# Kernel tuning notes

Measured on AMD Instinct MI355X. Metric: run time of the kernel, lower is better.

## Reference

```python
import jax, jax.numpy as jnp
import numpy as np

B, T, D, M, L = 4, 2048, 256, 128, 16
P = M * L  # max_pair_cnt


def setup_inputs() -> dict:
    key = jax.random.key(0)
    ks = jax.random.split(key, 11)
    head = jax.random.normal(ks[0], (B, P, T), jnp.float32) * 0.05
    tail = jax.random.normal(ks[1], (B, P, T), jnp.float32) * 0.05
    x = jax.random.normal(ks[2], (B, T, D), jnp.float32)
    coref_mention_position = jax.random.uniform(ks[3], (B, M, T), jnp.float32)
    lab = jax.random.uniform(ks[4], (B, P, 2), jnp.float32) + 1e-3
    coref_label = lab / lab.sum(-1, keepdims=True)  # already-softmaxed target
    coref_label_mask = jax.random.randint(ks[5], (B, P), 0, 2).astype(bool)
    lens = jnp.full((B, M), L, jnp.int32)  # uniform segment lengths
    w1 = jax.random.normal(ks[6], (3 * D, D), jnp.float32) / np.sqrt(3 * D).astype(np.float32)
    b1 = jnp.zeros((D,), jnp.float32)
    w2 = jax.random.normal(ks[7], (D, 2), jnp.float32) / np.sqrt(D).astype(np.float32)
    b2 = jnp.zeros((2,), jnp.float32)
    return {"head": head, "tail": tail, "lens": lens, "x": x,
            "coref_mention_position": coref_mention_position,
            "coref_label": coref_label, "coref_label_mask": coref_label_mask,
            "w1": w1, "b1": b1, "w2": w2, "b2": b2}


def reference(head, tail, lens, x, coref_mention_position, coref_label,
              coref_label_mask, w1, b1, w2, b2):
    # bmm-based gather of mention reps: [B,P,T] @ [B,T,D] -> [B,P,D]
    head_rep = jnp.einsum('bpt,btd->bpd', head, x)
    tail_rep = jnp.einsum('bpt,btd->bpd', tail, x)
    feat = jnp.concatenate([head_rep, tail_rep, head_rep * tail_rep], axis=-1)
    logits = jax.nn.relu(feat @ w1 + b1) @ w2 + b2  # [B,P,2]

    # ragged split_n_pad -> per-mention top-1 select (uniform lens == L -> reshape)
    scores = logits[..., 1].reshape(B, M, L)            # [B,M,L]
    max_idx = jnp.argmax(scores, axis=-1)               # [B,M]
    max_val = jnp.max(scores, axis=-1)                  # [B,M] (raw logit, as in source)
    tail_seg = tail_rep.reshape(B, M, L, D)
    sel = jnp.take_along_axis(tail_seg, max_idx[:, :, None, None], axis=2)[:, :, 0, :]
    coref_rep_m = sel * max_val[:, :, None]             # [B,M,D]

    # scatter-bmm merge back into sequence: [B,T,M] @ [B,M,D] -> [B,T,D]
    coref_rep = jnp.einsum('bmt,bmd->btd', coref_mention_position, coref_rep_m)
    output = x + coref_rep

    # KLDivLoss(reduction='mean') over masked pairs
    logq = jax.nn.log_softmax(logits, axis=-1)
    lab = coref_label
    pw = jnp.where(lab > 0, lab * jnp.log(jnp.maximum(lab, 1e-38)), 0.0) - lab * logq
    n = jnp.sum(coref_label_mask).astype(jnp.float32)
    loss = jnp.where(coref_label_mask[..., None], pw, 0.0).sum() / (n * 2.0)
    return output, loss
```

## Files before the change

kernel.cpp:

```cpp
#include <hip/hip_runtime.h>
#include <hip/hip_bf16.h>
#include <stdint.h>

#define TAU 0.35f

typedef __attribute__((ext_vector_type(8))) short bf16x8;
typedef __attribute__((ext_vector_type(4))) float f32x4;

__device__ __forceinline__ unsigned short f2bf(float f) {
  __bf16 h = (__bf16)f;
  return __builtin_bit_cast(unsigned short, h);
}
__device__ __forceinline__ float bf2f(unsigned short u) {
  unsigned int v = ((unsigned int)u) << 16;
  return __builtin_bit_cast(float, v);
}
__device__ __forceinline__ void async_copy16(const void* g, void* l) {
  __builtin_amdgcn_global_load_lds(
      (const __attribute__((address_space(1))) unsigned int*)g,
      (__attribute__((address_space(3))) unsigned int*)l, 16, 0, 0);
}

__global__ __launch_bounds__(256) void k_prep(
    const float* __restrict__ x, const float* __restrict__ w1,
    const float* __restrict__ b2,
    unsigned short* __restrict__ xt, unsigned short* __restrict__ w1t,
    float* __restrict__ logits, int* __restrict__ njobs) {
  __shared__ float tileS[64][65];
  int bx = blockIdx.x, tid = threadIdx.x;
  if (bx == 0 && tid == 0) *njobs = 0;
  if (bx < 64) {
    int i = bx * 256 + tid;
    logits[i] = b2[i & 1];
  }
  int j = tid & 63, i0 = tid >> 6;
  if (bx < 512) {
    int b = bx >> 7, t6 = (bx >> 2) & 31, d6 = bx & 3;
    const float* src = x + ((size_t)b * 2048 + (size_t)t6 * 64) * 256 + d6 * 64;
    for (int i = i0; i < 64; i += 4) tileS[i][j] = src[(size_t)i * 256 + j];
    __syncthreads();
    unsigned short* dst = xt + ((size_t)b * 256 + (size_t)d6 * 64) * 2048 + t6 * 64;
    for (int r = i0; r < 64; r += 4) dst[(size_t)r * 2048 + j] = f2bf(tileS[j][r]);
  } else {
    int wt = bx - 512;
    int k6 = wt >> 2, n6 = wt & 3;
    const float* src = w1 + ((size_t)k6 * 64) * 256 + n6 * 64;
    for (int i = i0; i < 64; i += 4) tileS[i][j] = src[(size_t)i * 256 + j];
    __syncthreads();
    unsigned short* dst = w1t + ((size_t)n6 * 64) * 768 + k6 * 64;
    for (int r = i0; r < 64; r += 4) dst[(size_t)r * 768 + j] = f2bf(tileS[j][r]);
  }
}

__global__ __launch_bounds__(256, 4) void k_gemm_rep(
    const float* __restrict__ head, const float* __restrict__ tail,
    const unsigned short* __restrict__ xt,
    float* __restrict__ hrep, float* __restrict__ trep) {
  __shared__ unsigned short As[2][4096];
  __shared__ unsigned short Bs[2][4096];
  int bx = blockIdx.x;
  int ntile = bx >> 8;
  int g = bx & 255;
  int b = g >> 6, mtile = g & 63;
  const float* Asrc = ((mtile < 32) ? head : tail) +
                      ((size_t)(b * 2048 + (mtile & 31) * 64)) * 2048;
  float* Crep = (mtile < 32) ? hrep : trep;
  const unsigned short* Bsrc = xt + ((size_t)(b * 256 + ntile * 64)) * 2048;

  int tid = threadIdx.x, lane = tid & 63, w = tid >> 6;

  int arow = tid >> 2, akq = tid & 3;
  const float* aptr = Asrc + (size_t)arow * 2048 + akq * 16;
  int rt = arow >> 4, r15 = arow & 15;
  int k8a = akq * 2, k8b = akq * 2 + 1;
  int awi0 = rt * 128 + (k8a >> 2) * 64 + (k8a & 3) * 16 + r15;
  int awi1 = rt * 128 + (k8b >> 2) * 64 + (k8b & 3) * 16 + r15;

  const unsigned short* bg[2];
  int bdst[2];
#pragma unroll
  for (int a = 0; a < 2; ++a) {
    int colofs = a * 8 + (lane >> 3);
    int k8 = (lane & 7) ^ (colofs & 7);
    bg[a] = Bsrc + (size_t)(w * 16 + colofs) * 2048 + k8 * 8;
    bdst[a] = (w * 128 + a * 64 + lane) * 8;
  }

  int sw0 = (lane >> 4) ^ (lane & 7);
  int sw1 = (4 + (lane >> 4)) ^ (lane & 7);
  int colc[4];
#pragma unroll
  for (int ct = 0; ct < 4; ++ct) colc[ct] = (ct * 16 + (lane & 15)) * 8;

  f32x4 acc[4];
#pragma unroll
  for (int ct = 0; ct < 4; ++ct) acc[ct] = (f32x4){0.f, 0.f, 0.f, 0.f};

  float4 av[4];
  {
    const float4* ap = (const float4*)aptr;
    av[0] = ap[0]; av[1] = ap[1]; av[2] = ap[2]; av[3] = ap[3];
  }
#pragma unroll
  for (int a = 0; a < 2; ++a) { async_copy16(bg[a], &Bs[0][bdst[a]]); bg[a] += 64; }
  {
    bf16x8 p0, p1;
    p0[0] = (short)f2bf(av[0].x); p0[1] = (short)f2bf(av[0].y);
    p0[2] = (short)f2bf(av[0].z); p0[3] = (short)f2bf(av[0].w);
    p0[4] = (short)f2bf(av[1].x); p0[5] = (short)f2bf(av[1].y);
    p0[6] = (short)f2bf(av[1].z); p0[7] = (short)f2bf(av[1].w);
    p1[0] = (short)f2bf(av[2].x); p1[1] = (short)f2bf(av[2].y);
    p1[2] = (short)f2bf(av[2].z); p1[3] = (short)f2bf(av[2].w);
    p1[4] = (short)f2bf(av[3].x); p1[5] = (short)f2bf(av[3].y);
    p1[6] = (short)f2bf(av[3].z); p1[7] = (short)f2bf(av[3].w);
    *(bf16x8*)&As[0][awi0 * 8] = p0;
    *(bf16x8*)&As[0][awi1 * 8] = p1;
  }
  {
    const float4* ap = (const float4*)(aptr + 64);
    av[0] = ap[0]; av[1] = ap[1]; av[2] = ap[2]; av[3] = ap[3];
  }
  __syncthreads();

  for (int it = 0; it < 32; ++it) {
    int cur = it & 1, nxt = cur ^ 1;
    if (it < 31) {
#pragma unroll
      for (int a = 0; a < 2; ++a) { async_copy16(bg[a], &Bs[nxt][bdst[a]]); bg[a] += 64; }
      bf16x8 p0, p1;
      p0[0] = (short)f2bf(av[0].x); p0[1] = (short)f2bf(av[0].y);
      p0[2] = (short)f2bf(av[0].z); p0[3] = (short)f2bf(av[0].w);
      p0[4] = (short)f2bf(av[1].x); p0[5] = (short)f2bf(av[1].y);
      p0[6] = (short)f2bf(av[1].z); p0[7] = (short)f2bf(av[1].w);
      p1[0] = (short)f2bf(av[2].x); p1[1] = (short)f2bf(av[2].y);
      p1[2] = (short)f2bf(av[2].z); p1[3] = (short)f2bf(av[2].w);
      p1[4] = (short)f2bf(av[3].x); p1[5] = (short)f2bf(av[3].y);
      p1[6] = (short)f2bf(av[3].z); p1[7] = (short)f2bf(av[3].w);
      *(bf16x8*)&As[nxt][awi0 * 8] = p0;
      *(bf16x8*)&As[nxt][awi1 * 8] = p1;
    }
    if (it < 30) {
      const float4* ap = (const float4*)(aptr + (it + 2) * 64);
      av[0] = ap[0]; av[1] = ap[1]; av[2] = ap[2]; av[3] = ap[3];
    }
    const unsigned short* A_ = As[cur];
    const unsigned short* B_ = Bs[cur];
    bf16x8 a0 = *(const bf16x8*)&A_[(w * 128 + lane) * 8];
    bf16x8 a1 = *(const bf16x8*)&A_[(w * 128 + 64 + lane) * 8];
#pragma unroll
    for (int ct = 0; ct < 4; ++ct) {
      bf16x8 b0 = *(const bf16x8*)&B_[(colc[ct] + sw0) * 8];
      acc[ct] = __builtin_amdgcn_mfma_f32_16x16x32_bf16(a0, b0, acc[ct], 0, 0, 0);
    }
#pragma unroll
    for (int ct = 0; ct < 4; ++ct) {
      bf16x8 b1 = *(const bf16x8*)&B_[(colc[ct] + sw1) * 8];
      acc[ct] = __builtin_amdgcn_mfma_f32_16x16x32_bf16(a1, b1, acc[ct], 0, 0, 0);
    }
    __syncthreads();
  }

  size_t prow = (size_t)b * 2048 + (size_t)(mtile & 31) * 64 + w * 16 + ((lane >> 4) << 2);
  int cb = ntile * 64 + (lane & 15);
#pragma unroll
  for (int ct = 0; ct < 4; ++ct)
#pragma unroll
    for (int i = 0; i < 4; ++i)
      Crep[(prow + i) * 256 + cb + ct * 16] = acc[ct][i];
}

__global__ __launch_bounds__(256) void k_feat(
    const float* __restrict__ hrep, const float* __restrict__ trep,
    unsigned short* __restrict__ featbf) {
  int gid = blockIdx.x * 256 + threadIdx.x;
  int p = gid >> 6, d0 = (gid & 63) * 4;
  float4 h4 = *(const float4*)&hrep[(size_t)p * 256 + d0];
  float4 t4 = *(const float4*)&trep[(size_t)p * 256 + d0];
  ushort4 a, bb, c;
  a.x = f2bf(h4.x); a.y = f2bf(h4.y); a.z = f2bf(h4.z); a.w = f2bf(h4.w);
  bb.x = f2bf(t4.x); bb.y = f2bf(t4.y); bb.z = f2bf(t4.z); bb.w = f2bf(t4.w);
  c.x = f2bf(h4.x * t4.x); c.y = f2bf(h4.y * t4.y);
  c.z = f2bf(h4.z * t4.z); c.w = f2bf(h4.w * t4.w);
  *(ushort4*)&featbf[(size_t)p * 768 + d0] = a;
  *(ushort4*)&featbf[(size_t)p * 768 + 256 + d0] = bb;
  *(ushort4*)&featbf[(size_t)p * 768 + 512 + d0] = c;
}

__global__ __launch_bounds__(256, 4) void k_gemm_mlp(
    const unsigned short* __restrict__ featb, const unsigned short* __restrict__ w1t,
    const float* __restrict__ b1, const float* __restrict__ w2,
    float* __restrict__ logits) {
  __shared__ unsigned short As[2][4096], Bs[2][4096];
  int bx = blockIdx.x;
  int ntile = bx >> 7;
  int mtile = bx & 127;
  int tid = threadIdx.x, lane = tid & 63, w = tid >> 6;

  const unsigned short* ag[2];
  const unsigned short* bgp[2];
  int dofs[2];
#pragma unroll
  for (int a = 0; a < 2; ++a) {
    int rowofs = a * 8 + (lane >> 3);
    int k8 = (lane & 7) ^ (rowofs & 7);
    ag[a] = featb + (size_t)(mtile * 64 + w * 16 + rowofs) * 768 + k8 * 8;
    bgp[a] = w1t + (size_t)(ntile * 64 + w * 16 + rowofs) * 768 + k8 * 8;
    dofs[a] = (w * 128 + a * 64 + lane) * 8;
  }
  int sw0 = (lane >> 4) ^ (lane & 7);
  int sw1 = (4 + (lane >> 4)) ^ (lane & 7);
  int arowc = (w * 16 + (lane & 15)) * 8;
  int colc[4];
#pragma unroll
  for (int ct = 0; ct < 4; ++ct) colc[ct] = (ct * 16 + (lane & 15)) * 8;

  f32x4 acc[4];
#pragma unroll
  for (int ct = 0; ct < 4; ++ct) acc[ct] = (f32x4){0.f, 0.f, 0.f, 0.f};

#pragma unroll
  for (int a = 0; a < 2; ++a) {
    async_copy16(ag[a], &As[0][dofs[a]]); ag[a] += 64;
    async_copy16(bgp[a], &Bs[0][dofs[a]]); bgp[a] += 64;
  }
  __syncthreads();

  for (int it = 0; it < 12; ++it) {
    int cur = it & 1, nxt = cur ^ 1;
    if (it < 11) {
#pragma unroll
      for (int a = 0; a < 2; ++a) {
        async_copy16(ag[a], &As[nxt][dofs[a]]); ag[a] += 64;
        async_copy16(bgp[a], &Bs[nxt][dofs[a]]); bgp[a] += 64;
      }
    }
    const unsigned short* A_ = As[cur];
    const unsigned short* B_ = Bs[cur];
    bf16x8 a0 = *(const bf16x8*)&A_[(arowc + sw0) * 8];
    bf16x8 a1 = *(const bf16x8*)&A_[(arowc + sw1) * 8];
#pragma unroll
    for (int ct = 0; ct < 4; ++ct) {
      bf16x8 b0 = *(const bf16x8*)&B_[(colc[ct] + sw0) * 8];
      acc[ct] = __builtin_amdgcn_mfma_f32_16x16x32_bf16(a0, b0, acc[ct], 0, 0, 0);
    }
#pragma unroll
    for (int ct = 0; ct < 4; ++ct) {
      bf16x8 b1 = *(const bf16x8*)&B_[(colc[ct] + sw1) * 8];
      acc[ct] = __builtin_amdgcn_mfma_f32_16x16x32_bf16(a1, b1, acc[ct], 0, 0, 0);
    }
    __syncthreads();
  }

  float bv[4], w20[4], w21[4];
#pragma unroll
  for (int ct = 0; ct < 4; ++ct) {
    int col = ntile * 64 + ct * 16 + (lane & 15);
    bv[ct] = b1[col]; w20[ct] = w2[col * 2]; w21[ct] = w2[col * 2 + 1];
  }
#pragma unroll
  for (int i = 0; i < 4; ++i) {
    float s0 = 0.f, s1 = 0.f;
#pragma unroll
    for (int ct = 0; ct < 4; ++ct) {
      float r = fmaxf(acc[ct][i] + bv[ct], 0.f);
      s0 += r * w20[ct]; s1 += r * w21[ct];
    }
#pragma unroll
    for (int off = 1; off < 16; off <<= 1) {
      s0 += __shfl_xor(s0, off); s1 += __shfl_xor(s1, off);
    }
    if ((lane & 15) == 0) {
      int row = mtile * 64 + w * 16 + ((lane >> 4) << 2) + i;
      atomicAdd(&logits[row * 2], s0);
      atomicAdd(&logits[row * 2 + 1], s1);
    }
  }
}

__global__ void k_select(const float* __restrict__ logits, int* __restrict__ idxv,
                         float* __restrict__ mval, int* __restrict__ cmask,
                         int* __restrict__ njobs, int* __restrict__ jobs) {
  int q = blockIdx.x * 256 + threadIdx.x;
  if (q >= 512) return;
  int base = q * 16;
  float s[16];
#pragma unroll
  for (int i = 0; i < 16; ++i) s[i] = logits[(size_t)(base + i) * 2 + 1];
  float best = s[0]; int bi = 0;
#pragma unroll
  for (int i = 1; i < 16; ++i) if (s[i] > best) { best = s[i]; bi = i; }
  int mask = 0, cnt = 0;
#pragma unroll
  for (int i = 0; i < 16; ++i) if (s[i] > best - TAU) { mask |= 1 << i; ++cnt; }
  idxv[q] = bi; mval[q] = best;
  if (cnt > 1) {
    cmask[q] = mask;
    for (int i = 0; i < 16; ++i)
      if ((mask >> i) & 1) { int j = atomicAdd(njobs, 1); jobs[j] = base + i; }
  } else cmask[q] = 0;
}

__global__ __launch_bounds__(1024) void k_refine(
    const int* __restrict__ njobs, const int* __restrict__ jobs,
    const float* __restrict__ head, const float* __restrict__ tail,
    const float* __restrict__ x, const float* __restrict__ w1,
    const float* __restrict__ b1, const float* __restrict__ w2,
    const float* __restrict__ b2, float* __restrict__ refined) {
  __shared__ float hrow[2048], trow[2048], feat[768], red[1024], red2[1024];
  int tid = threadIdx.x, seg = tid >> 8, d = tid & 255;
  int nj = *njobs;
  for (int job = blockIdx.x; job < nj; job += gridDim.x) {
    int code = jobs[job];
    int b = code >> 11, p = code & 2047;
    if (tid < 512)
      *(float4*)&hrow[tid * 4] = *(const float4*)&head[((size_t)(b * 2048 + p)) * 2048 + tid * 4];
    else {
      int u = tid - 512;
      *(float4*)&trow[u * 4] = *(const float4*)&tail[((size_t)(b * 2048 + p)) * 2048 + u * 4];
    }
    __syncthreads();
    float hr = 0.f, tr = 0.f;
    const float* xb = x + ((size_t)b * 2048) * 256 + d;
#pragma unroll 8
    for (int t = seg * 512; t < seg * 512 + 512; ++t) {
      float xv = xb[(size_t)t * 256];
      hr += hrow[t] * xv; tr += trow[t] * xv;
    }
    red[tid] = hr; red2[tid] = tr;
    __syncthreads();
    if (seg == 0) {
      float fh = red[d] + red[256 + d] + red[512 + d] + red[768 + d];
      float ft = red2[d] + red2[256 + d] + red2[512 + d] + red2[768 + d];
      feat[d] = fh; feat[256 + d] = ft; feat[512 + d] = fh * ft;
    }
    __syncthreads();
    float hp = 0.f;
    for (int ii = seg * 192; ii < seg * 192 + 192; ++ii) hp += feat[ii] * w1[(size_t)ii * 256 + d];
    red[tid] = hp;
    __syncthreads();
    if (seg == 0) {
      float hj = b1[d] + red[d] + red[256 + d] + red[512 + d] + red[768 + d];
      hj = fmaxf(hj, 0.f);
      red2[d] = hj * w2[d * 2 + 1];
    }
    __syncthreads();
    for (int s = 128; s > 0; s >>= 1) {
      if (tid < s) red2[tid] += red2[tid + s];
      __syncthreads();
    }
    if (tid == 0) refined[code] = red2[0] + b2[1];
    __syncthreads();
  }
}

__global__ __launch_bounds__(256) void k_repm(
    const int* __restrict__ idxv, const float* __restrict__ mval,
    const int* __restrict__ cmask, const float* __restrict__ refined,
    const float* __restrict__ trep, float* __restrict__ repm) {
  int q = blockIdx.x, d = threadIdx.x;
  int mask = cmask[q]; int bi; float v;
  if (mask) {
    bi = -1; v = -1e30f;
    for (int i = 0; i < 16; ++i)
      if ((mask >> i) & 1) { float s = refined[q * 16 + i]; if (s > v) { v = s; bi = i; } }
  } else { bi = idxv[q]; v = mval[q]; }
  repm[(size_t)q * 256 + d] = trep[((size_t)q * 16 + bi) * 256 + d] * v;
}

__global__ __launch_bounds__(256) void k_merge(
    const float* __restrict__ cmp, const float* __restrict__ repm,
    const float* __restrict__ x, float* __restrict__ out) {
  __shared__ float cl[128 * 16];
  int bx = blockIdx.x, b = bx >> 7, t0 = (bx & 127) * 16;
  int tid = threadIdx.x;
#pragma unroll
  for (int it = 0; it < 2; ++it) {
    int f = it * 256 + tid;
    int row = f >> 2, c4 = (f & 3) * 4;
    *(float4*)&cl[row * 16 + c4] =
        *(const float4*)&cmp[((size_t)(b * 128 + row)) * 2048 + t0 + c4];
  }
  __syncthreads();
  float acc[16];
#pragma unroll
  for (int i = 0; i < 16; ++i) acc[i] = 0.f;
  int d = tid;
  for (int m = 0; m < 128; ++m) {
    float rv = repm[(size_t)(b * 128 + m) * 256 + d];
    const float4* c4p = (const float4*)&cl[m * 16];
#pragma unroll
    for (int jj = 0; jj < 4; ++jj) {
      float4 c = c4p[jj];
      acc[jj * 4] += c.x * rv; acc[jj * 4 + 1] += c.y * rv;
      acc[jj * 4 + 2] += c.z * rv; acc[jj * 4 + 3] += c.w * rv;
    }
  }
  const float* xb = x + ((size_t)(b * 2048 + t0)) * 256 + d;
  float* ob = out + ((size_t)(b * 2048 + t0)) * 256 + d;
#pragma unroll
  for (int tt = 0; tt < 16; ++tt) ob[(size_t)tt * 256] = xb[(size_t)tt * 256] + acc[tt];
}

__global__ __launch_bounds__(1024) void k_loss(
    const float* __restrict__ logits, const float* __restrict__ lab,
    const unsigned char* __restrict__ mask, float* __restrict__ out_loss) {
  __shared__ float rs[1024], rc[1024];
  int tid = threadIdx.x;
  float sum = 0.f, cnt = 0.f;
  for (int p = tid; p < 8192; p += 1024) {
    float l0 = logits[(size_t)p * 2], l1 = logits[(size_t)p * 2 + 1];
    float a0 = lab[(size_t)p * 2], a1 = lab[(size_t)p * 2 + 1];
    float mx = fmaxf(l0, l1);
    float lse = mx + logf(expf(l0 - mx) + expf(l1 - mx));
    float pw = 0.f;
    if (a0 > 0.f) pw += a0 * logf(fmaxf(a0, 1e-38f));
    if (a1 > 0.f) pw += a1 * logf(fmaxf(a1, 1e-38f));
    pw -= a0 * (l0 - lse) + a1 * (l1 - lse);
    if (mask[p]) { sum += pw; cnt += 1.f; }
  }
  rs[tid] = sum; rc[tid] = cnt;
  __syncthreads();
  for (int s = 512; s > 0; s >>= 1) {
    if (tid < s) { rs[tid] += rs[tid + s]; rc[tid] += rc[tid + s]; }
    __syncthreads();
  }
  if (tid == 0) *out_loss = rs[0] / (rc[0] * 2.0f);
}

extern "C" void kernel_launch(void* const* d_in, const int* in_sizes, int n_in,
                              void* d_out, int out_size, void* d_ws, size_t ws_size,
                              hipStream_t stream) {
  (void)in_sizes; (void)n_in; (void)out_size; (void)ws_size;
  const float* head = (const float*)d_in[0];
  const float* tail = (const float*)d_in[1];
  const float* x = (const float*)d_in[3];
  const float* cmp = (const float*)d_in[4];
  const float* lab = (const float*)d_in[5];
  const unsigned char* lmask = (const unsigned char*)d_in[6];
  const float* w1 = (const float*)d_in[7];
  const float* b1 = (const float*)d_in[8];
  const float* w2 = (const float*)d_in[9];
  const float* b2 = (const float*)d_in[10];
  float* out = (float*)d_out;

  char* ws = (char*)d_ws;
  size_t off = 0;
  auto alloc = [&](size_t bytes) -> void* {
    void* p = ws + off; off += (bytes + 255) & ~(size_t)255; return p;
  };
  unsigned short* xt = (unsigned short*)alloc(4ull * 256 * 2048 * 2);
  unsigned short* w1t = (unsigned short*)alloc(256ull * 768 * 2);
  float* hrep = (float*)alloc(8192ull * 256 * 4);
  float* trep = (float*)alloc(8192ull * 256 * 4);
  unsigned short* featb = (unsigned short*)alloc(8192ull * 768 * 2);
  float* logits = (float*)alloc(8192ull * 2 * 4);
  float* refined = (float*)alloc(8192ull * 4);
  int* idxv = (int*)alloc(512 * 4);
  float* mvalv = (float*)alloc(512 * 4);
  int* cmaskv = (int*)alloc(512 * 4);
  int* njobs = (int*)alloc(256);
  int* jobs = (int*)alloc(8192 * 4);
  float* repm = (float*)alloc(512ull * 256 * 4);

  k_prep<<<560, 256, 0, stream>>>(x, w1, b2, xt, w1t, logits, njobs);
  k_gemm_rep<<<1024, 256, 0, stream>>>(head, tail, xt, hrep, trep);
  k_feat<<<2048, 256, 0, stream>>>(hrep, trep, featb);
  k_gemm_mlp<<<512, 256, 0, stream>>>(featb, w1t, b1, w2, logits);
  k_select<<<2, 256, 0, stream>>>(logits, idxv, mvalv, cmaskv, njobs, jobs);
  k_refine<<<256, 1024, 0, stream>>>(njobs, jobs, head, tail, x, w1, b1, w2, b2, refined);
  k_repm<<<512, 256, 0, stream>>>(idxv, mvalv, cmaskv, refined, trep, repm);
  k_merge<<<512, 256, 0, stream>>>(cmp, repm, x, out);
  k_loss<<<1, 1024, 0, stream>>>(logits, lab, lmask, out + 4ull * 2048 * 256);
}
```

Baseline: 330.4 us.

## Switch GEMMs to fp16 MFMA, tighten refine threshold, restructure LDS staging

Replaces bf16 with fp16 for the staged operands and MFMA instructions in both GEMM kernels, and lowers the TAU threshold that decides which near-tie pairs get recomputed in fp32 by the refine kernel. The higher fp16 mantissa precision is meant to allow fewer refine jobs. The LDS layout is changed to unswizzled per-lane row copies, and the A-tile fp16 pack/write is moved after the MFMAs so it overlaps with compute. Risks include fp16 range limits, LDS bank conflicts from dropping the XOR swizzle, and argmax mismatches if the smaller TAU misses true ties.

```diff
diff --git a/kernel.cpp b/kernel.cpp
--- a/kernel.cpp
+++ b/kernel.cpp
@@ -2,18 +2,14 @@
 #include <hip/hip_bf16.h>
 #include <stdint.h>
 
-#define TAU 0.35f
-
-typedef __attribute__((ext_vector_type(8))) short bf16x8;
+#define TAU 0.05f
+
+typedef __attribute__((ext_vector_type(8))) _Float16 f16x8;
 typedef __attribute__((ext_vector_type(4))) float f32x4;
 
-__device__ __forceinline__ unsigned short f2bf(float f) {
-  __bf16 h = (__bf16)f;
+__device__ __forceinline__ unsigned short f2h(float f) {
+  _Float16 h = (_Float16)f;
   return __builtin_bit_cast(unsigned short, h);
-}
-__device__ __forceinline__ float bf2f(unsigned short u) {
-  unsigned int v = ((unsigned int)u) << 16;
-  return __builtin_bit_cast(float, v);
 }
 __device__ __forceinline__ void async_copy16(const void* g, void* l) {
   __builtin_amdgcn_global_load_lds(
@@ -40,7 +36,7 @@
     for (int i = i0; i < 64; i += 4) tileS[i][j] = src[(size_t)i * 256 + j];
     __syncthreads();
     unsigned short* dst = xt + ((size_t)b * 256 + (size_t)d6 * 64) * 2048 + t6 * 64;
-    for (int r = i0; r < 64; r += 4) dst[(size_t)r * 2048 + j] = f2bf(tileS[j][r]);
+    for (int r = i0; r < 64; r += 4) dst[(size_t)r * 2048 + j] = f2h(tileS[j][r]);
   } else {
     int wt = bx - 512;
     int k6 = wt >> 2, n6 = wt & 3;
@@ -48,7 +44,7 @@
     for (int i = i0; i < 64; i += 4) tileS[i][j] = src[(size_t)i * 256 + j];
     __syncthreads();
     unsigned short* dst = w1t + ((size_t)n6 * 64) * 768 + k6 * 64;
-    for (int r = i0; r < 64; r += 4) dst[(size_t)r * 768 + j] = f2bf(tileS[j][r]);
+    for (int r = i0; r < 64; r += 4) dst[(size_t)r * 768 + j] = f2h(tileS[j][r]);
   }
 }
 
@@ -68,100 +64,90 @@
   const unsigned short* Bsrc = xt + ((size_t)(b * 256 + ntile * 64)) * 2048;
 
   int tid = threadIdx.x, lane = tid & 63, w = tid >> 6;
-
-  int arow = tid >> 2, akq = tid & 3;
-  const float* aptr = Asrc + (size_t)arow * 2048 + akq * 16;
-  int rt = arow >> 4, r15 = arow & 15;
-  int k8a = akq * 2, k8b = akq * 2 + 1;
-  int awi0 = rt * 128 + (k8a >> 2) * 64 + (k8a & 3) * 16 + r15;
-  int awi1 = rt * 128 + (k8b >> 2) * 64 + (k8b & 3) * 16 + r15;
-
-  const unsigned short* bg[2];
-  int bdst[2];
-#pragma unroll
-  for (int a = 0; a < 2; ++a) {
-    int colofs = a * 8 + (lane >> 3);
-    int k8 = (lane & 7) ^ (colofs & 7);
-    bg[a] = Bsrc + (size_t)(w * 16 + colofs) * 2048 + k8 * 8;
-    bdst[a] = (w * 128 + a * 64 + lane) * 8;
-  }
-
-  int sw0 = (lane >> 4) ^ (lane & 7);
-  int sw1 = (4 + (lane >> 4)) ^ (lane & 7);
-  int colc[4];
-#pragma unroll
-  for (int ct = 0; ct < 4; ++ct) colc[ct] = (ct * 16 + (lane & 15)) * 8;
+  int l15 = lane & 15, l4 = lane >> 4;
+
+  const float* aptr = Asrc + (size_t)(w * 16 + l15) * 2048 + l4 * 16;
+  int aw_chunk0 = (l4 * 2) * 64 + w * 16 + l15;
+  int aw_chunk1 = (l4 * 2 + 1) * 64 + w * 16 + l15;
+
+  const unsigned short* bg0 = Bsrc + (size_t)lane * 2048 + 2 * w * 8;
+  const unsigned short* bg1 = bg0 + 8;
+
+  int ac0 = ((0 + l4) * 64 + w * 16 + l15) * 8;
+  int ac1 = ((4 + l4) * 64 + w * 16 + l15) * 8;
+  int bc[2][4];
+#pragma unroll
+  for (int kh = 0; kh < 2; ++kh)
+#pragma unroll
+    for (int ct = 0; ct < 4; ++ct)
+      bc[kh][ct] = ((kh * 4 + l4) * 64 + ct * 16 + l15) * 8;
 
   f32x4 acc[4];
 #pragma unroll
   for (int ct = 0; ct < 4; ++ct) acc[ct] = (f32x4){0.f, 0.f, 0.f, 0.f};
 
-  float4 av[4];
+  auto pack_write = [&](float4* av, unsigned short* Abuf) {
+    f16x8 p0, p1;
+    p0[0] = (_Float16)av[0].x; p0[1] = (_Float16)av[0].y;
+    p0[2] = (_Float16)av[0].z; p0[3] = (_Float16)av[0].w;
+    p0[4] = (_Float16)av[1].x; p0[5] = (_Float16)av[1].y;
+    p0[6] = (_Float16)av[1].z; p0[7] = (_Float16)av[1].w;
+    p1[0] = (_Float16)av[2].x; p1[1] = (_Float16)av[2].y;
+    p1[2] = (_Float16)av[2].z; p1[3] = (_Float16)av[2].w;
+    p1[4] = (_Float16)av[3].x; p1[5] = (_Float16)av[3].y;
+    p1[6] = (_Float16)av[3].z; p1[7] = (_Float16)av[3].w;
+    *(f16x8*)&Abuf[aw_chunk0 * 8] = p0;
+    *(f16x8*)&Abuf[aw_chunk1 * 8] = p1;
+  };
+
+  float4 avW[4], avF[4];
   {
     const float4* ap = (const float4*)aptr;
-    av[0] = ap[0]; av[1] = ap[1]; av[2] = ap[2]; av[3] = ap[3];
-  }
-#pragma unroll
-  for (int a = 0; a < 2; ++a) { async_copy16(bg[a], &Bs[0][bdst[a]]); bg[a] += 64; }
-  {
-    bf16x8 p0, p1;
-    p0[0] = (short)f2bf(av[0].x); p0[1] = (short)f2bf(av[0].y);
-    p0[2] = (short)f2bf(av[0].z); p0[3] = (short)f2bf(av[0].w);
-    p0[4] = (short)f2bf(av[1].x); p0[5] = (short)f2bf(av[1].y);
-    p0[6] = (short)f2bf(av[1].z); p0[7] = (short)f2bf(av[1].w);
-    p1[0] = (short)f2bf(av[2].x); p1[1] = (short)f2bf(av[2].y);
-    p1[2] = (short)f2bf(av[2].z); p1[3] = (short)f2bf(av[2].w);
-    p1[4] = (short)f2bf(av[3].x); p1[5] = (short)f2bf(av[3].y);
-    p1[6] = (short)f2bf(av[3].z); p1[7] = (short)f2bf(av[3].w);
-    *(bf16x8*)&As[0][awi0 * 8] = p0;
-    *(bf16x8*)&As[0][awi1 * 8] = p1;
-  }
+    avW[0] = ap[0]; avW[1] = ap[1]; avW[2] = ap[2]; avW[3] = ap[3];
+  }
+  async_copy16(bg0, &Bs[0][(2 * w * 64) * 8]);
+  async_copy16(bg1, &Bs[0][((2 * w + 1) * 64) * 8]);
+  pack_write(avW, As[0]);
   {
     const float4* ap = (const float4*)(aptr + 64);
-    av[0] = ap[0]; av[1] = ap[1]; av[2] = ap[2]; av[3] = ap[3];
+    avW[0] = ap[0]; avW[1] = ap[1]; avW[2] = ap[2]; avW[3] = ap[3];
   }
   __syncthreads();
 
   for (int it = 0; it < 32; ++it) {
     int cur = it & 1, nxt = cur ^ 1;
     if (it < 31) {
-#pragma unroll
-      for (int a = 0; a < 2; ++a) { async_copy16(bg[a], &Bs[nxt][bdst[a]]); bg[a] += 64; }
-      bf16x8 p0, p1;
-      p0[0] = (short)f2bf(av[0].x); p0[1] = (short)f2bf(av[0].y);
-      p0[2] = (short)f2bf(av[0].z); p0[3] = (short)f2bf(av[0].w);
-      p0[4] = (short)f2bf(av[1].x); p0[5] = (short)f2bf(av[1].y);
-      p0[6] = (short)f2bf(av[1].z); p0[7] = (short)f2bf(av[1].w);
-      p1[0] = (short)f2bf(av[2].x); p1[1] = (short)f2bf(av[2].y);
-      p1[2] = (short)f2bf(av[2].z); p1[3] = (short)f2bf(av[2].w);
-      p1[4] = (short)f2bf(av[3].x); p1[5] = (short)f2bf(av[3].y);
-      p1[6] = (short)f2bf(av[3].z); p1[7] = (short)f2bf(av[3].w);
-      *(bf16x8*)&As[nxt][awi0 * 8] = p0;
-      *(bf16x8*)&As[nxt][awi1 * 8] = p1;
+      const unsigned short* g0 = Bsrc + (size_t)lane * 2048 + (it + 1) * 64 + 2 * w * 8;
+      async_copy16(g0, &Bs[nxt][(2 * w * 64) * 8]);
+      async_copy16(g0 + 8, &Bs[nxt][((2 * w + 1) * 64) * 8]);
     }
     if (it < 30) {
       const float4* ap = (const float4*)(aptr + (it + 2) * 64);
-      av[0] = ap[0]; av[1] = ap[1]; av[2] = ap[2]; av[3] = ap[3];
+      avF[0] = ap[0]; avF[1] = ap[1]; avF[2] = ap[2]; avF[3] = ap[3];
     }
     const unsigned short* A_ = As[cur];
     const unsigned short* B_ = Bs[cur];
-    bf16x8 a0 = *(const bf16x8*)&A_[(w * 128 + lane) * 8];
-    bf16x8 a1 = *(const bf16x8*)&A_[(w * 128 + 64 + lane) * 8];
+    f16x8 a0 = *(const f16x8*)&A_[ac0];
+    f16x8 a1 = *(const f16x8*)&A_[ac1];
 #pragma unroll
     for (int ct = 0; ct < 4; ++ct) {
-      bf16x8 b0 = *(const bf16x8*)&B_[(colc[ct] + sw0) * 8];
-      acc[ct] = __builtin_amdgcn_mfma_f32_16x16x32_bf16(a0, b0, acc[ct], 0, 0, 0);
+      f16x8 b0 = *(const f16x8*)&B_[bc[0][ct]];
+      acc[ct] = __builtin_amdgcn_mfma_f32_16x16x32_f16(a0, b0, acc[ct], 0, 0, 0);
     }
 #pragma unroll
     for (int ct = 0; ct < 4; ++ct) {
-      bf16x8 b1 = *(const bf16x8*)&B_[(colc[ct] + sw1) * 8];
-      acc[ct] = __builtin_amdgcn_mfma_f32_16x16x32_bf16(a1, b1, acc[ct], 0, 0, 0);
-    }
-    __syncthreads();
-  }
-
-  size_t prow = (size_t)b * 2048 + (size_t)(mtile & 31) * 64 + w * 16 + ((lane >> 4) << 2);
-  int cb = ntile * 64 + (lane & 15);
+      f16x8 b1 = *(const f16x8*)&B_[bc[1][ct]];
+      acc[ct] = __builtin_amdgcn_mfma_f32_16x16x32_f16(a1, b1, acc[ct], 0, 0, 0);
+    }
+    if (it < 31) {
+      pack_write(avW, As[nxt]);
+      avW[0] = avF[0]; avW[1] = avF[1]; avW[2] = avF[2]; avW[3] = avF[3];
+    }
+    __syncthreads();
+  }
+
+  size_t prow = (size_t)b * 2048 + (size_t)(mtile & 31) * 64 + w * 16 + l4 * 4;
+  int cb = ntile * 64 + l15;
 #pragma unroll
   for (int ct = 0; ct < 4; ++ct)
 #pragma unroll
@@ -171,23 +157,23 @@
 
 __global__ __launch_bounds__(256) void k_feat(
     const float* __restrict__ hrep, const float* __restrict__ trep,
-    unsigned short* __restrict__ featbf) {
+    unsigned short* __restrict__ featf) {
   int gid = blockIdx.x * 256 + threadIdx.x;
   int p = gid >> 6, d0 = (gid & 63) * 4;
   float4 h4 = *(const float4*)&hrep[(size_t)p * 256 + d0];
   float4 t4 = *(const float4*)&trep[(size_t)p * 256 + d0];
   ushort4 a, bb, c;
-  a.x = f2bf(h4.x); a.y = f2bf(h4.y); a.z = f2bf(h4.z); a.w = f2bf(h4.w);
-  bb.x = f2bf(t4.x); bb.y = f2bf(t4.y); bb.z = f2bf(t4.z); bb.w = f2bf(t4.w);
-  c.x = f2bf(h4.x * t4.x); c.y = f2bf(h4.y * t4.y);
-  c.z = f2bf(h4.z * t4.z); c.w = f2bf(h4.w * t4.w);
-  *(ushort4*)&featbf[(size_t)p * 768 + d0] = a;
-  *(ushort4*)&featbf[(size_t)p * 768 + 256 + d0] = bb;
-  *(ushort4*)&featbf[(size_t)p * 768 + 512 + d0] = c;
+  a.x = f2h(h4.x); a.y = f2h(h4.y); a.z = f2h(h4.z); a.w = f2h(h4.w);
+  bb.x = f2h(t4.x); bb.y = f2h(t4.y); bb.z = f2h(t4.z); bb.w = f2h(t4.w);
+  c.x = f2h(h4.x * t4.x); c.y = f2h(h4.y * t4.y);
+  c.z = f2h(h4.z * t4.z); c.w = f2h(h4.w * t4.w);
+  *(ushort4*)&featf[(size_t)p * 768 + d0] = a;
+  *(ushort4*)&featf[(size_t)p * 768 + 256 + d0] = bb;
+  *(ushort4*)&featf[(size_t)p * 768 + 512 + d0] = c;
 }
 
 __global__ __launch_bounds__(256, 4) void k_gemm_mlp(
-    const unsigned short* __restrict__ featb, const unsigned short* __restrict__ w1t,
+    const unsigned short* __restrict__ featf, const unsigned short* __restrict__ w1t,
     const float* __restrict__ b1, const float* __restrict__ w2,
     float* __restrict__ logits) {
   __shared__ unsigned short As[2][4096], Bs[2][4096];
@@ -195,58 +181,53 @@
   int ntile = bx >> 7;
   int mtile = bx & 127;
   int tid = threadIdx.x, lane = tid & 63, w = tid >> 6;
-
-  const unsigned short* ag[2];
-  const unsigned short* bgp[2];
-  int dofs[2];
-#pragma unroll
-  for (int a = 0; a < 2; ++a) {
-    int rowofs = a * 8 + (lane >> 3);
-    int k8 = (lane & 7) ^ (rowofs & 7);
-    ag[a] = featb + (size_t)(mtile * 64 + w * 16 + rowofs) * 768 + k8 * 8;
-    bgp[a] = w1t + (size_t)(ntile * 64 + w * 16 + rowofs) * 768 + k8 * 8;
-    dofs[a] = (w * 128 + a * 64 + lane) * 8;
-  }
-  int sw0 = (lane >> 4) ^ (lane & 7);
-  int sw1 = (4 + (lane >> 4)) ^ (lane & 7);
-  int arowc = (w * 16 + (lane & 15)) * 8;
-  int colc[4];
-#pragma unroll
-  for (int ct = 0; ct < 4; ++ct) colc[ct] = (ct * 16 + (lane & 15)) * 8;
+  int l15 = lane & 15, l4 = lane >> 4;
+
+  const unsigned short* Ag = featf + (size_t)(mtile * 64 + lane) * 768 + 2 * w * 8;
+  const unsigned short* Bg = w1t + (size_t)(ntile * 64 + lane) * 768 + 2 * w * 8;
+
+  int ac0 = ((0 + l4) * 64 + w * 16 + l15) * 8;
+  int ac1 = ((4 + l4) * 64 + w * 16 + l15) * 8;
+  int bc[2][4];
+#pragma unroll
+  for (int kh = 0; kh < 2; ++kh)
+#pragma unroll
+    for (int ct = 0; ct < 4; ++ct)
+      bc[kh][ct] = ((kh * 4 + l4) * 64 + ct * 16 + l15) * 8;
 
   f32x4 acc[4];
 #pragma unroll
   for (int ct = 0; ct < 4; ++ct) acc[ct] = (f32x4){0.f, 0.f, 0.f, 0.f};
 
-#pragma unroll
-  for (int a = 0; a < 2; ++a) {
-    async_copy16(ag[a], &As[0][dofs[a]]); ag[a] += 64;
-    async_copy16(bgp[a], &Bs[0][dofs[a]]); bgp[a] += 64;
-  }
+  async_copy16(Ag, &As[0][(2 * w * 64) * 8]);
+  async_copy16(Ag + 8, &As[0][((2 * w + 1) * 64) * 8]);
+  async_copy16(Bg, &Bs[0][(2 * w * 64) * 8]);
+  async_copy16(Bg + 8, &Bs[0][((2 * w + 1) * 64) * 8]);
   __syncthreads();
 
   for (int it = 0; it < 12; ++it) {
     int cur = it & 1, nxt = cur ^ 1;
     if (it < 11) {
-#pragma unroll
-      for (int a = 0; a < 2; ++a) {
-        async_copy16(ag[a], &As[nxt][dofs[a]]); ag[a] += 64;
-        async_copy16(bgp[a], &Bs[nxt][dofs[a]]); bgp[a] += 64;
-      }
+      const unsigned short* ga = Ag + (it + 1) * 64;
+      const unsigned short* gb = Bg + (it + 1) * 64;
+      async_copy16(ga, &As[nxt][(2 * w * 64) * 8]);
+      async_copy16(ga + 8, &As[nxt][((2 * w + 1) * 64) * 8]);
+      async_copy16(gb, &Bs[nxt][(2 * w * 64) * 8]);
+      async_copy16(gb + 8, &Bs[nxt][((2 * w + 1) * 64) * 8]);
     }
     const unsigned short* A_ = As[cur];
     const unsigned short* B_ = Bs[cur];
-    bf16x8 a0 = *(const bf16x8*)&A_[(arowc + sw0) * 8];
-    bf16x8 a1 = *(const bf16x8*)&A_[(arowc + sw1) * 8];
+    f16x8 a0 = *(const f16x8*)&A_[ac0];
+    f16x8 a1 = *(const f16x8*)&A_[ac1];
 #pragma unroll
     for (int ct = 0; ct < 4; ++ct) {
-      bf16x8 b0 = *(const bf16x8*)&B_[(colc[ct] + sw0) * 8];
-      acc[ct] = __builtin_amdgcn_mfma_f32_16x16x32_bf16(a0, b0, acc[ct], 0, 0, 0);
+      f16x8 b0 = *(const f16x8*)&B_[bc[0][ct]];
+      acc[ct] = __builtin_amdgcn_mfma_f32_16x16x32_f16(a0, b0, acc[ct], 0, 0, 0);
     }
 #pragma unroll
     for (int ct = 0; ct < 4; ++ct) {
-      bf16x8 b1 = *(const bf16x8*)&B_[(colc[ct] + sw1) * 8];
-      acc[ct] = __builtin_amdgcn_mfma_f32_16x16x32_bf16(a1, b1, acc[ct], 0, 0, 0);
+      f16x8 b1 = *(const f16x8*)&B_[bc[1][ct]];
+      acc[ct] = __builtin_amdgcn_mfma_f32_16x16x32_f16(a1, b1, acc[ct], 0, 0, 0);
     }
     __syncthreads();
   }
@@ -254,7 +235,7 @@
   float bv[4], w20[4], w21[4];
 #pragma unroll
   for (int ct = 0; ct < 4; ++ct) {
-    int col = ntile * 64 + ct * 16 + (lane & 15);
+    int col = ntile * 64 + ct * 16 + l15;
     bv[ct] = b1[col]; w20[ct] = w2[col * 2]; w21[ct] = w2[col * 2 + 1];
   }
 #pragma unroll
@@ -269,8 +250,8 @@
     for (int off = 1; off < 16; off <<= 1) {
       s0 += __shfl_xor(s0, off); s1 += __shfl_xor(s1, off);
     }
-    if ((lane & 15) == 0) {
-      int row = mtile * 64 + w * 16 + ((lane >> 4) << 2) + i;
+    if (l15 == 0) {
+      int row = mtile * 64 + w * 16 + l4 * 4 + i;
       atomicAdd(&logits[row * 2], s0);
       atomicAdd(&logits[row * 2 + 1], s1);
     }
@@ -452,7 +433,7 @@
   unsigned short* w1t = (unsigned short*)alloc(256ull * 768 * 2);
   float* hrep = (float*)alloc(8192ull * 256 * 4);
   float* trep = (float*)alloc(8192ull * 256 * 4);
-  unsigned short* featb = (unsigned short*)alloc(8192ull * 768 * 2);
+  unsigned short* featf = (unsigned short*)alloc(8192ull * 768 * 2);
   float* logits = (float*)alloc(8192ull * 2 * 4);
   float* refined = (float*)alloc(8192ull * 4);
   int* idxv = (int*)alloc(512 * 4);
@@ -464,8 +445,8 @@
 
   k_prep<<<560, 256, 0, stream>>>(x, w1, b2, xt, w1t, logits, njobs);
   k_gemm_rep<<<1024, 256, 0, stream>>>(head, tail, xt, hrep, trep);
-  k_feat<<<2048, 256, 0, stream>>>(hrep, trep, featb);
-  k_gemm_mlp<<<512, 256, 0, stream>>>(featb, w1t, b1, w2, logits);
+  k_feat<<<2048, 256, 0, stream>>>(hrep, trep, featf);
+  k_gemm_mlp<<<512, 256, 0, stream>>>(featf, w1t, b1, w2, logits);
   k_select<<<2, 256, 0, stream>>>(logits, idxv, mvalv, cmaskv, njobs, jobs);
   k_refine<<<256, 1024, 0, stream>>>(njobs, jobs, head, tail, x, w1, b1, w2, b2, refined);
   k_repm<<<512, 256, 0, stream>>>(idxv, mvalv, cmaskv, refined, trep, repm);
```

Result: no change. 334.6 us (+1.3%).
